# Optimization experiments

Hardware: AMD Instinct MI355X
Metric: run time of the kernel (lower is better)

## Reference

```python
import jax, jax.numpy as jnp
import numpy as np

B, W, H, C = 4, 32, 32, 128   # image feature map
S, D = 256, 512               # text seq len, text embed dim
NC = 64                       # num_channels (attention inner dim)


def setup_inputs() -> dict:
    key = jax.random.key(0)
    ks = jax.random.split(key, 16)
    def dense(k, din, dout):
        return jax.random.normal(k, (din, dout), jnp.float32) / np.sqrt(din)
    return {
        "x": jax.random.normal(ks[0], (B, W, H, C), jnp.float32),
        "s": jax.random.normal(ks[1], (B, S, D), jnp.float32),
        "a": jax.random.randint(ks[2], (B, S), 0, 2).astype(jnp.float32),
        "Wq": dense(ks[3], C, NC),  "bq": jnp.zeros((NC,), jnp.float32),
        "Wkx": dense(ks[4], C, NC), "bkx": jnp.zeros((NC,), jnp.float32),
        "Wvx": dense(ks[5], C, NC), "bvx": jnp.zeros((NC,), jnp.float32),
        "Wks": dense(ks[6], D, NC), "bks": jnp.zeros((NC,), jnp.float32),
        "Wvs": dense(ks[7], D, NC), "bvs": jnp.zeros((NC,), jnp.float32),
        "Wout": dense(ks[8], NC, C), "bout": jnp.zeros((C,), jnp.float32),
        "ln_scale": jnp.ones((C,), jnp.float32),
        "ln_bias": jnp.zeros((C,), jnp.float32),
    }


def reference(x, s, a, Wq, bq, Wkx, bkx, Wvx, bvx, Wks, bks, Wvs, bvs,
              Wout, bout, ln_scale, ln_bias):
    nc = Wq.shape[-1]
    # mask text embeddings: repeat(a,'b s -> b s d') * s
    te = s * a[:, :, None]
    # projections
    q = x @ Wq + bq            # (b,w,h,c)
    kx = x @ Wkx + bkx         # (b,w,h,c)
    vx = x @ Vx_dummy if False else x @ Wvx + bvx
    ks = te @ Wks + bks        # (b,s,c)
    vs = te @ Wvs + bvs        # (b,s,c)
    # broadcast-add spatial and text keys/values -> (b,w,h,s,c)
    k = kx[:, :, :, None, :] + ks[:, None, None, :, :]
    v = vx[:, :, :, None, :] + vs[:, None, None, :, :]
    # attention matrix over channels: v^T @ k contracted over s -> (b,w,h,c,c)
    attn = jnp.einsum('bwhsc,bwhsd->bwhcd', v, k) / jnp.sqrt(jnp.asarray(nc, x.dtype))
    attn = jax.nn.softmax(attn, axis=-1)
    # q applied through the channel-channel attention -> (b,w,h,c)
    out = jnp.einsum('bwhj,bwhjk->bwhk', q, attn)
    # output projection back to x channels, residual, layernorm
    out = out @ Wout + bout
    x = x + out
    mu = jnp.mean(x, axis=-1, keepdims=True)
    var = jnp.var(x, axis=-1, keepdims=True)
    x = (x - mu) * jax.lax.rsqrt(var + 1e-6) * ln_scale + ln_bias
    return x
```

## Files before the change

kernel.cpp:

```cpp
#include <hip/hip_runtime.h>
#include <hip/hip_bf16.h>

#define BB 4
#define SS 256
#define DD 512
#define CC 128
#define NC 64
#define PXB 4

__global__ __launch_bounds__(256) void fused_proj_kernel(
    const float* __restrict__ x,
    const float* __restrict__ Wq,  const float* __restrict__ bq,
    const float* __restrict__ Wkx, const float* __restrict__ bkx,
    const float* __restrict__ Wvx, const float* __restrict__ bvx,
    const float* __restrict__ s, const float* __restrict__ a,
    const float* __restrict__ Wks, const float* __restrict__ bks,
    const float* __restrict__ Wvs, const float* __restrict__ bvs,
    float* __restrict__ P, float* __restrict__ ksw, float* __restrict__ vsw)
{
    __shared__ float tel[2][DD];
    __shared__ float part[2][2][2][NC];
    __shared__ float xl[8][CC];

    const int t = threadIdx.x;
    const int w = t >> 6, lane = t & 63;

    if (blockIdx.x < 512) {
        const int px0 = blockIdx.x * 8;
        {
            const float4* x4 = (const float4*)(x + (size_t)px0 * CC);
            ((float4*)&xl[0][0])[t] = x4[t];
        }
        __syncthreads();
        if (w < 3) {
            const float* __restrict__ Wm = (w == 0) ? Wq : (w == 1 ? Wkx : Wvx);
            const float* __restrict__ bm = (w == 0) ? bq : (w == 1 ? bkx : bvx);
            const int ksub = lane >> 4;
            const int cg = (lane & 15) * 4;
            float4 acc[8] = {};
            #pragma unroll 4
            for (int j = 0; j < 32; ++j) {
                const int k = 4 * j + ksub;
                const float4 wv = *(const float4*)(Wm + (size_t)k * NC + cg);
                #pragma unroll
                for (int px = 0; px < 8; ++px) {
                    const float xv = xl[px][k];
                    acc[px].x = fmaf(xv, wv.x, acc[px].x);
                    acc[px].y = fmaf(xv, wv.y, acc[px].y);
                    acc[px].z = fmaf(xv, wv.z, acc[px].z);
                    acc[px].w = fmaf(xv, wv.w, acc[px].w);
                }
            }
            #pragma unroll
            for (int px = 0; px < 8; ++px) {
                #pragma unroll
                for (int off = 16; off <= 32; off <<= 1) {
                    acc[px].x += __shfl_down(acc[px].x, off);
                    acc[px].y += __shfl_down(acc[px].y, off);
                    acc[px].z += __shfl_down(acc[px].z, off);
                    acc[px].w += __shfl_down(acc[px].w, off);
                }
            }
            if (ksub == 0) {
                const float4 bb = *(const float4*)(bm + cg);
                #pragma unroll
                for (int px = 0; px < 8; ++px) {
                    float4 v;
                    v.x = acc[px].x + bb.x; v.y = acc[px].y + bb.y;
                    v.z = acc[px].z + bb.z; v.w = acc[px].w + bb.w;
                    *(float4*)(P + (size_t)(px0 + px) * 192 + w * 64 + cg) = v;
                }
            }
        }
    } else {
        const int row0 = (blockIdx.x - 512) * 2;
        {
            const float4* s4 = (const float4*)(s + (size_t)row0 * DD);
            const int r = t >> 7;
            const float am = a[row0 + r];
            float4 v = s4[t];
            v.x *= am; v.y *= am; v.z *= am; v.w *= am;
            ((float4*)&tel[0][0])[t] = v;
        }
        __syncthreads();

        const int m = w & 1, h = w >> 1;
        const int kb = h * 256;
        const int cg = (lane & 15) * 4;
        const int ksub = lane >> 4;
        const float* __restrict__ Wm = m ? Wvs : Wks;

        float4 acc0 = {0,0,0,0}, acc1 = {0,0,0,0};
        #pragma unroll 4
        for (int j = 0; j < 64; ++j) {
            const int k = kb + 4 * j + ksub;
            const float4 wv = *(const float4*)(Wm + (size_t)k * NC + cg);
            const float t0 = tel[0][k];
            const float t1 = tel[1][k];
            acc0.x = fmaf(t0, wv.x, acc0.x); acc0.y = fmaf(t0, wv.y, acc0.y);
            acc0.z = fmaf(t0, wv.z, acc0.z); acc0.w = fmaf(t0, wv.w, acc0.w);
            acc1.x = fmaf(t1, wv.x, acc1.x); acc1.y = fmaf(t1, wv.y, acc1.y);
            acc1.z = fmaf(t1, wv.z, acc1.z); acc1.w = fmaf(t1, wv.w, acc1.w);
        }
        #pragma unroll
        for (int off = 16; off <= 32; off <<= 1) {
            acc0.x += __shfl_down(acc0.x, off); acc0.y += __shfl_down(acc0.y, off);
            acc0.z += __shfl_down(acc0.z, off); acc0.w += __shfl_down(acc0.w, off);
            acc1.x += __shfl_down(acc1.x, off); acc1.y += __shfl_down(acc1.y, off);
            acc1.z += __shfl_down(acc1.z, off); acc1.w += __shfl_down(acc1.w, off);
        }
        if (lane < 16) {
            *(float4*)&part[m][h][0][cg] = acc0;
            *(float4*)&part[m][h][1][cg] = acc1;
        }
        __syncthreads();

        {
            const int mm = t >> 7, r = (t >> 6) & 1, col = t & 63;
            const float v = part[mm][0][r][col] + part[mm][1][r][col]
                          + (mm ? bvs[col] : bks[col]);
            float* dst = mm ? vsw : ksw;
            dst[(size_t)(row0 + r) * NC + col] = v;
        }
    }
}

__global__ __launch_bounds__(256) void reduce_kernel(
    const float* __restrict__ ksw, const float* __restrict__ vsw,
    float* __restrict__ Mw, float* __restrict__ Ksw, float* __restrict__ Vsw)
{
    __shared__ float pm[4][NC], pk[4][NC], pv[4];
    const int t = threadIdx.x, w = t >> 6, d = t & 63;
    const int b = blockIdx.x >> 6, c = blockIdx.x & 63;
    const float* __restrict__ vsb = vsw + (size_t)b * SS * NC;
    const float* __restrict__ ksb = ksw + (size_t)b * SS * NC;
    float acc = 0.f, ks_ = 0.f, vs_ = 0.f;
    #pragma unroll 4
    for (int j = 0; j < 64; ++j) {
        const int s2 = w * 64 + j;
        const float vv = vsb[s2 * NC + c];
        const float kv = ksb[s2 * NC + d];
        acc = fmaf(vv, kv, acc);
        ks_ += kv; vs_ += vv;
    }
    pm[w][d] = acc; pk[w][d] = ks_;
    if (d == 0) pv[w] = vs_;
    __syncthreads();
    if (t < 64) {
        Mw[((size_t)b * NC + c) * NC + t] = pm[0][t] + pm[1][t] + pm[2][t] + pm[3][t];
        if (c == 0) Ksw[b * NC + t] = pk[0][t] + pk[1][t] + pk[2][t] + pk[3][t];
        if (t == 0) Vsw[b * NC + c] = pv[0] + pv[1] + pv[2] + pv[3];
    }
}

__global__ __launch_bounds__(256) void pixel_kernel(
    const float* __restrict__ x, const float* __restrict__ P,
    const float* __restrict__ Wout, const float* __restrict__ bout,
    const float* __restrict__ ln_scale, const float* __restrict__ ln_bias,
    const float* __restrict__ Mw, const float* __restrict__ Ksw,
    const float* __restrict__ Vsw,
    float* __restrict__ out)
{
    __shared__ float Ml[NC * 65];
    __shared__ float projl[PXB][192];
    __shared__ float xl[PXB][CC];
    __shared__ float rsl[PXB][NC];
    __shared__ float mxl[PXB][NC];
    __shared__ float outl[PXB][NC];
    __shared__ float Ksl[NC], Vsl[NC];
    __shared__ float redl[2][2][4];

    const int t = threadIdx.x;
    const int w = t >> 6, lane = t & 63;
    const int px0g = blockIdx.x * PXB;
    const int b = px0g >> 10;

    {
        const float4* P4 = (const float4*)(P + (size_t)px0g * 192);
        for (int i = t; i < PXB * 192 / 4; i += 256)
            ((float4*)&projl[0][0])[i] = P4[i];
        const float4* x4 = (const float4*)(x + (size_t)px0g * CC);
        for (int i = t; i < PXB * CC / 4; i += 256)
            ((float4*)&xl[0][0])[i] = x4[i];
        const float* Mb = Mw + (size_t)b * NC * NC;
        for (int i = t; i < NC * NC; i += 256)
            Ml[(i >> 6) * 65 + (i & 63)] = Mb[i];
        if (t < NC) { Ksl[t] = Ksw[b * NC + t]; Vsl[t] = Vsw[b * NC + t]; }
    }
    __syncthreads();

    {
        const int px = w, c = lane;
        const float vxc = projl[px][128 + c];
        const float qc  = projl[px][c];
        const float uc  = fmaf(256.0f, vxc, Vsl[c]);
        float mx = -3.4e38f;
        #pragma unroll
        for (int d = 0; d < NC; ++d) {
            const float A = fmaf(uc, projl[px][64 + d],
                                 fmaf(vxc, Ksl[d], Ml[c * 65 + d])) * 0.125f;
            mx = fmaxf(mx, A);
        }
        float sum = 0.f;
        #pragma unroll
        for (int d = 0; d < NC; ++d) {
            const float A = fmaf(uc, projl[px][64 + d],
                                 fmaf(vxc, Ksl[d], Ml[c * 65 + d])) * 0.125f;
            sum += __expf(A - mx);
        }
        rsl[px][c] = qc / sum;
        mxl[px][c] = mx;
    }
    __syncthreads();

    {
        const int px = w, d = lane;
        const float kxd = projl[px][64 + d];
        const float Ksd = Ksl[d];
        float acc = 0.f;
        #pragma unroll 4
        for (int c = 0; c < NC; ++c) {
            const float vxc = projl[px][128 + c];
            const float uc = fmaf(256.0f, vxc, Vsl[c]);
            const float A = fmaf(uc, kxd, fmaf(vxc, Ksd, Ml[c * 65 + d])) * 0.125f;
            acc = fmaf(rsl[px][c], __expf(A - mxl[px][c]), acc);
        }
        outl[px][d] = acc;
    }
    __syncthreads();

    {
        const int col = t & 127;
        const int pxg = t >> 7;
        const int px0 = 2 * pxg, px1 = px0 + 1;
        float acc0 = 0.f, acc1 = 0.f;
        #pragma unroll 4
        for (int k = 0; k < NC; ++k) {
            const float wv = Wout[k * CC + col];
            acc0 = fmaf(outl[px0][k], wv, acc0);
            acc1 = fmaf(outl[px1][k], wv, acc1);
        }
        const float bb = bout[col];
        const float y0 = acc0 + bb + xl[px0][col];
        const float y1 = acc1 + bb + xl[px1][col];

        float s10 = y0, s20 = y0 * y0, s11 = y1, s21 = y1 * y1;
        #pragma unroll
        for (int off = 32; off >= 1; off >>= 1) {
            s10 += __shfl_down(s10, off);
            s20 += __shfl_down(s20, off);
            s11 += __shfl_down(s11, off);
            s21 += __shfl_down(s21, off);
        }
        const int half = (t >> 6) & 1;
        if (lane == 0) {
            redl[pxg][half][0] = s10; redl[pxg][half][1] = s20;
            redl[pxg][half][2] = s11; redl[pxg][half][3] = s21;
        }
        __syncthreads();
        const float S10 = redl[pxg][0][0] + redl[pxg][1][0];
        const float S20 = redl[pxg][0][1] + redl[pxg][1][1];
        const float S11 = redl[pxg][0][2] + redl[pxg][1][2];
        const float S21 = redl[pxg][0][3] + redl[pxg][1][3];
        const float mu0 = S10 * (1.f / 128.f);
        const float var0 = S20 * (1.f / 128.f) - mu0 * mu0;
        const float mu1 = S11 * (1.f / 128.f);
        const float var1 = S21 * (1.f / 128.f) - mu1 * mu1;
        const float r0 = rsqrtf(var0 + 1e-6f), r1 = rsqrtf(var1 + 1e-6f);
        const float gg = ln_scale[col], be = ln_bias[col];
        out[(size_t)(px0g + px0) * CC + col] = (y0 - mu0) * r0 * gg + be;
        out[(size_t)(px0g + px1) * CC + col] = (y1 - mu1) * r1 * gg + be;
    }
}

extern "C" void kernel_launch(void* const* d_in, const int* in_sizes, int n_in,
                              void* d_out, int out_size, void* d_ws, size_t ws_size,
                              hipStream_t stream) {
    const float* x        = (const float*)d_in[0];
    const float* s        = (const float*)d_in[1];
    const float* a        = (const float*)d_in[2];
    const float* Wq       = (const float*)d_in[3];
    const float* bq       = (const float*)d_in[4];
    const float* Wkx      = (const float*)d_in[5];
    const float* bkx      = (const float*)d_in[6];
    const float* Wvx      = (const float*)d_in[7];
    const float* bvx      = (const float*)d_in[8];
    const float* Wks      = (const float*)d_in[9];
    const float* bks      = (const float*)d_in[10];
    const float* Wvs      = (const float*)d_in[11];
    const float* bvs      = (const float*)d_in[12];
    const float* Wout     = (const float*)d_in[13];
    const float* bout     = (const float*)d_in[14];
    const float* ln_scale = (const float*)d_in[15];
    const float* ln_bias  = (const float*)d_in[16];

    float* ws  = (float*)d_ws;
    float* ksw = ws;
    float* vsw = ws + 65536;
    float* Mw  = ws + 131072;
    float* Ksw = ws + 147456;
    float* Vsw = ws + 147712;
    float* Pw  = ws + 147968;

    fused_proj_kernel<<<1024, 256, 0, stream>>>(
        x, Wq, bq, Wkx, bkx, Wvx, bvx, s, a, Wks, bks, Wvs, bvs, Pw, ksw, vsw);
    reduce_kernel<<<BB * NC, 256, 0, stream>>>(ksw, vsw, Mw, Ksw, Vsw);
    pixel_kernel<<<(BB * 1024) / PXB, 256, 0, stream>>>(
        x, Pw, Wout, bout, ln_scale, ln_bias, Mw, Ksw, Vsw, (float*)d_out);
}
```

Measured before the change: 117.1 us.

## Fuse pixel projections into pixel kernel and compute text M partials per block

The change restructures three launches into two. The text kernel now projects 16 text rows per block and writes partial M, Ks and Vs sums, which removes the separate reduce kernel. The pixel kernel computes q/kx/vx projections in shared memory, so the P workspace no longer goes through global memory, and it sums the 16 M partials itself. The costs are that every pixel block redundantly sums 16 partials of 64x64 floats, the text stage runs on only 64 blocks, and the pixel grid shrinks to 256 blocks of 1024 threads.

```diff
diff --git a/kernel.cpp b/kernel.cpp
--- a/kernel.cpp
+++ b/kernel.cpp
@@ -1,191 +1,204 @@
 #include <hip/hip_runtime.h>
-#include <hip/hip_bf16.h>
 
 #define BB 4
 #define SS 256
 #define DD 512
 #define CC 128
 #define NC 64
-#define PXB 4
-
-__global__ __launch_bounds__(256) void fused_proj_kernel(
+
+__global__ __launch_bounds__(512) void text_kernel(
+    const float* __restrict__ s, const float* __restrict__ a,
+    const float* __restrict__ Wks, const float* __restrict__ bks,
+    const float* __restrict__ Wvs, const float* __restrict__ bvs,
+    float* __restrict__ Mpart, float* __restrict__ Kspart,
+    float* __restrict__ Vspart)
+{
+    __shared__ float tel[16][DD];
+    __shared__ float ksl[16][NC];
+    __shared__ float vsl[16][NC];
+
+    const int t = threadIdx.x;
+    const int w = t >> 6, lane = t & 63;
+    const int b = blockIdx.x >> 4, q = blockIdx.x & 15;
+    const int srow0 = b * SS + q * 16;
+
+    {
+        const float4* s4 = (const float4*)(s + (size_t)srow0 * DD);
+        for (int i = t; i < 2048; i += 512) {
+            const int r = i >> 7;
+            const float am = a[srow0 + r];
+            float4 v = s4[i];
+            v.x *= am; v.y *= am; v.z *= am; v.w *= am;
+            ((float4*)&tel[0][0])[i] = v;
+        }
+    }
+    __syncthreads();
+
+    {
+        const int m = w & 1, rg = w >> 1;
+        const float* __restrict__ Wm = m ? Wvs : Wks;
+        const float* __restrict__ bm = m ? bvs : bks;
+        const int ksub = lane >> 4;
+        const int cg = (lane & 15) * 4;
+        float4 acc[4] = {};
+        #pragma unroll 4
+        for (int j = 0; j < 128; ++j) {
+            const int k = 4 * j + ksub;
+            const float4 wv = *(const float4*)(Wm + (size_t)k * NC + cg);
+            #pragma unroll
+            for (int r = 0; r < 4; ++r) {
+                const float tv = tel[rg * 4 + r][k];
+                acc[r].x = fmaf(tv, wv.x, acc[r].x);
+                acc[r].y = fmaf(tv, wv.y, acc[r].y);
+                acc[r].z = fmaf(tv, wv.z, acc[r].z);
+                acc[r].w = fmaf(tv, wv.w, acc[r].w);
+            }
+        }
+        #pragma unroll
+        for (int off = 16; off <= 32; off <<= 1) {
+            #pragma unroll
+            for (int r = 0; r < 4; ++r) {
+                acc[r].x += __shfl_down(acc[r].x, off);
+                acc[r].y += __shfl_down(acc[r].y, off);
+                acc[r].z += __shfl_down(acc[r].z, off);
+                acc[r].w += __shfl_down(acc[r].w, off);
+            }
+        }
+        if (ksub == 0) {
+            const float4 bb = *(const float4*)(bm + cg);
+            float (*dst)[NC] = m ? vsl : ksl;
+            #pragma unroll
+            for (int r = 0; r < 4; ++r) {
+                float4 v;
+                v.x = acc[r].x + bb.x; v.y = acc[r].y + bb.y;
+                v.z = acc[r].z + bb.z; v.w = acc[r].w + bb.w;
+                *(float4*)&dst[rg * 4 + r][cg] = v;
+            }
+        }
+    }
+    __syncthreads();
+
+    {
+        const int c = t >> 3;
+        const int d0 = (t & 7) * 8;
+        float4 A0 = {0,0,0,0}, A1 = {0,0,0,0};
+        #pragma unroll
+        for (int ss = 0; ss < 16; ++ss) {
+            const float vv = vsl[ss][c];
+            const float4 k0 = *(const float4*)&ksl[ss][d0];
+            const float4 k1 = *(const float4*)&ksl[ss][d0 + 4];
+            A0.x = fmaf(vv, k0.x, A0.x); A0.y = fmaf(vv, k0.y, A0.y);
+            A0.z = fmaf(vv, k0.z, A0.z); A0.w = fmaf(vv, k0.w, A0.w);
+            A1.x = fmaf(vv, k1.x, A1.x); A1.y = fmaf(vv, k1.y, A1.y);
+            A1.z = fmaf(vv, k1.z, A1.z); A1.w = fmaf(vv, k1.w, A1.w);
+        }
+        float* Mp = Mpart + ((size_t)(b * 16 + q)) * (NC * NC) + c * NC + d0;
+        *(float4*)Mp = A0;
+        *(float4*)(Mp + 4) = A1;
+    }
+    if (t < 128) {
+        const int m = t >> 6, d = t & 63;
+        const float (*src)[NC] = m ? vsl : ksl;
+        float sum = 0.f;
+        #pragma unroll
+        for (int ss = 0; ss < 16; ++ss) sum += src[ss][d];
+        float* dst = m ? Vspart : Kspart;
+        dst[(b * 16 + q) * NC + d] = sum;
+    }
+}
+
+__global__ __launch_bounds__(1024) void pixel_kernel(
     const float* __restrict__ x,
     const float* __restrict__ Wq,  const float* __restrict__ bq,
     const float* __restrict__ Wkx, const float* __restrict__ bkx,
     const float* __restrict__ Wvx, const float* __restrict__ bvx,
-    const float* __restrict__ s, const float* __restrict__ a,
-    const float* __restrict__ Wks, const float* __restrict__ bks,
-    const float* __restrict__ Wvs, const float* __restrict__ bvs,
-    float* __restrict__ P, float* __restrict__ ksw, float* __restrict__ vsw)
+    const float* __restrict__ Wout, const float* __restrict__ bout,
+    const float* __restrict__ ln_scale, const float* __restrict__ ln_bias,
+    const float* __restrict__ Mpart, const float* __restrict__ Kspart,
+    const float* __restrict__ Vspart,
+    float* __restrict__ out)
 {
-    __shared__ float tel[2][DD];
-    __shared__ float part[2][2][2][NC];
-    __shared__ float xl[8][CC];
+    __shared__ float Ml[NC * 65];
+    __shared__ float projl[16][192];
+    __shared__ float xl[16][CC];
+    __shared__ float rsl[16][NC];
+    __shared__ float mxl[16][NC];
+    __shared__ float outl[16][NC];
+    __shared__ float Ksl[NC], Vsl[NC];
+    __shared__ float redl[8][2][4];
 
     const int t = threadIdx.x;
     const int w = t >> 6, lane = t & 63;
-
-    if (blockIdx.x < 512) {
-        const int px0 = blockIdx.x * 8;
-        {
-            const float4* x4 = (const float4*)(x + (size_t)px0 * CC);
-            ((float4*)&xl[0][0])[t] = x4[t];
-        }
-        __syncthreads();
-        if (w < 3) {
-            const float* __restrict__ Wm = (w == 0) ? Wq : (w == 1 ? Wkx : Wvx);
-            const float* __restrict__ bm = (w == 0) ? bq : (w == 1 ? bkx : bvx);
+    const int px0g = blockIdx.x * 16;
+    const int b = blockIdx.x >> 6;
+
+    if (t < 512)
+        ((float4*)&xl[0][0])[t] = ((const float4*)(x + (size_t)px0g * CC))[t];
+
+    {
+        const float4* Mp4 = (const float4*)(Mpart + (size_t)b * 16 * (NC * NC));
+        float4 acc = {0,0,0,0};
+        #pragma unroll
+        for (int q = 0; q < 16; ++q) {
+            const float4 v = Mp4[q * 1024 + t];
+            acc.x += v.x; acc.y += v.y; acc.z += v.z; acc.w += v.w;
+        }
+        const int c = t >> 4, dq = t & 15;
+        float* dst = &Ml[c * 65 + dq * 4];
+        dst[0] = acc.x; dst[1] = acc.y; dst[2] = acc.z; dst[3] = acc.w;
+    }
+    if (t < 128) {
+        const int m = t >> 6, d = t & 63;
+        const float* Pp = (m ? Vspart : Kspart) + b * 16 * NC + d;
+        float sum = 0.f;
+        #pragma unroll
+        for (int q = 0; q < 16; ++q) sum += Pp[q * NC];
+        (m ? Vsl : Ksl)[d] = sum;
+    }
+    __syncthreads();
+
+    {
+        const int g = w >> 2, mg = w & 3;
+        if (mg < 3) {
+            const float* __restrict__ Wm = (mg == 0) ? Wq : (mg == 1 ? Wkx : Wvx);
+            const float* __restrict__ bm = (mg == 0) ? bq : (mg == 1 ? bkx : bvx);
             const int ksub = lane >> 4;
             const int cg = (lane & 15) * 4;
-            float4 acc[8] = {};
+            float4 acc[4] = {};
             #pragma unroll 4
             for (int j = 0; j < 32; ++j) {
                 const int k = 4 * j + ksub;
                 const float4 wv = *(const float4*)(Wm + (size_t)k * NC + cg);
                 #pragma unroll
-                for (int px = 0; px < 8; ++px) {
-                    const float xv = xl[px][k];
-                    acc[px].x = fmaf(xv, wv.x, acc[px].x);
-                    acc[px].y = fmaf(xv, wv.y, acc[px].y);
-                    acc[px].z = fmaf(xv, wv.z, acc[px].z);
-                    acc[px].w = fmaf(xv, wv.w, acc[px].w);
+                for (int p = 0; p < 4; ++p) {
+                    const float xv = xl[g * 4 + p][k];
+                    acc[p].x = fmaf(xv, wv.x, acc[p].x);
+                    acc[p].y = fmaf(xv, wv.y, acc[p].y);
+                    acc[p].z = fmaf(xv, wv.z, acc[p].z);
+                    acc[p].w = fmaf(xv, wv.w, acc[p].w);
                 }
             }
             #pragma unroll
-            for (int px = 0; px < 8; ++px) {
+            for (int p = 0; p < 4; ++p) {
                 #pragma unroll
                 for (int off = 16; off <= 32; off <<= 1) {
-                    acc[px].x += __shfl_down(acc[px].x, off);
-                    acc[px].y += __shfl_down(acc[px].y, off);
-                    acc[px].z += __shfl_down(acc[px].z, off);
-                    acc[px].w += __shfl_down(acc[px].w, off);
+                    acc[p].x += __shfl_down(acc[p].x, off);
+                    acc[p].y += __shfl_down(acc[p].y, off);
+                    acc[p].z += __shfl_down(acc[p].z, off);
+                    acc[p].w += __shfl_down(acc[p].w, off);
                 }
             }
             if (ksub == 0) {
                 const float4 bb = *(const float4*)(bm + cg);
                 #pragma unroll
-                for (int px = 0; px < 8; ++px) {
+                for (int p = 0; p < 4; ++p) {
                     float4 v;
-                    v.x = acc[px].x + bb.x; v.y = acc[px].y + bb.y;
-                    v.z = acc[px].z + bb.z; v.w = acc[px].w + bb.w;
-                    *(float4*)(P + (size_t)(px0 + px) * 192 + w * 64 + cg) = v;
+                    v.x = acc[p].x + bb.x; v.y = acc[p].y + bb.y;
+                    v.z = acc[p].z + bb.z; v.w = acc[p].w + bb.w;
+                    *(float4*)&projl[g * 4 + p][mg * 64 + cg] = v;
                 }
             }
         }
-    } else {
-        const int row0 = (blockIdx.x - 512) * 2;
-        {
-            const float4* s4 = (const float4*)(s + (size_t)row0 * DD);
-            const int r = t >> 7;
-            const float am = a[row0 + r];
-            float4 v = s4[t];
-            v.x *= am; v.y *= am; v.z *= am; v.w *= am;
-            ((float4*)&tel[0][0])[t] = v;
-        }
-        __syncthreads();
-
-        const int m = w & 1, h = w >> 1;
-        const int kb = h * 256;
-        const int cg = (lane & 15) * 4;
-        const int ksub = lane >> 4;
-        const float* __restrict__ Wm = m ? Wvs : Wks;
-
-        float4 acc0 = {0,0,0,0}, acc1 = {0,0,0,0};
-        #pragma unroll 4
-        for (int j = 0; j < 64; ++j) {
-            const int k = kb + 4 * j + ksub;
-            const float4 wv = *(const float4*)(Wm + (size_t)k * NC + cg);
-            const float t0 = tel[0][k];
-            const float t1 = tel[1][k];
-            acc0.x = fmaf(t0, wv.x, acc0.x); acc0.y = fmaf(t0, wv.y, acc0.y);
-            acc0.z = fmaf(t0, wv.z, acc0.z); acc0.w = fmaf(t0, wv.w, acc0.w);
-            acc1.x = fmaf(t1, wv.x, acc1.x); acc1.y = fmaf(t1, wv.y, acc1.y);
-            acc1.z = fmaf(t1, wv.z, acc1.z); acc1.w = fmaf(t1, wv.w, acc1.w);
-        }
-        #pragma unroll
-        for (int off = 16; off <= 32; off <<= 1) {
-            acc0.x += __shfl_down(acc0.x, off); acc0.y += __shfl_down(acc0.y, off);
-            acc0.z += __shfl_down(acc0.z, off); acc0.w += __shfl_down(acc0.w, off);
-            acc1.x += __shfl_down(acc1.x, off); acc1.y += __shfl_down(acc1.y, off);
-            acc1.z += __shfl_down(acc1.z, off); acc1.w += __shfl_down(acc1.w, off);
-        }
-        if (lane < 16) {
-            *(float4*)&part[m][h][0][cg] = acc0;
-            *(float4*)&part[m][h][1][cg] = acc1;
-        }
-        __syncthreads();
-
-        {
-            const int mm = t >> 7, r = (t >> 6) & 1, col = t & 63;
-            const float v = part[mm][0][r][col] + part[mm][1][r][col]
-                          + (mm ? bvs[col] : bks[col]);
-            float* dst = mm ? vsw : ksw;
-            dst[(size_t)(row0 + r) * NC + col] = v;
-        }
-    }
-}
-
-__global__ __launch_bounds__(256) void reduce_kernel(
-    const float* __restrict__ ksw, const float* __restrict__ vsw,
-    float* __restrict__ Mw, float* __restrict__ Ksw, float* __restrict__ Vsw)
-{
-    __shared__ float pm[4][NC], pk[4][NC], pv[4];
-    const int t = threadIdx.x, w = t >> 6, d = t & 63;
-    const int b = blockIdx.x >> 6, c = blockIdx.x & 63;
-    const float* __restrict__ vsb = vsw + (size_t)b * SS * NC;
-    const float* __restrict__ ksb = ksw + (size_t)b * SS * NC;
-    float acc = 0.f, ks_ = 0.f, vs_ = 0.f;
-    #pragma unroll 4
-    for (int j = 0; j < 64; ++j) {
-        const int s2 = w * 64 + j;
-        const float vv = vsb[s2 * NC + c];
-        const float kv = ksb[s2 * NC + d];
-        acc = fmaf(vv, kv, acc);
-        ks_ += kv; vs_ += vv;
-    }
-    pm[w][d] = acc; pk[w][d] = ks_;
-    if (d == 0) pv[w] = vs_;
-    __syncthreads();
-    if (t < 64) {
-        Mw[((size_t)b * NC + c) * NC + t] = pm[0][t] + pm[1][t] + pm[2][t] + pm[3][t];
-        if (c == 0) Ksw[b * NC + t] = pk[0][t] + pk[1][t] + pk[2][t] + pk[3][t];
-        if (t == 0) Vsw[b * NC + c] = pv[0] + pv[1] + pv[2] + pv[3];
-    }
-}
-
-__global__ __launch_bounds__(256) void pixel_kernel(
-    const float* __restrict__ x, const float* __restrict__ P,
-    const float* __restrict__ Wout, const float* __restrict__ bout,
-    const float* __restrict__ ln_scale, const float* __restrict__ ln_bias,
-    const float* __restrict__ Mw, const float* __restrict__ Ksw,
-    const float* __restrict__ Vsw,
-    float* __restrict__ out)
-{
-    __shared__ float Ml[NC * 65];
-    __shared__ float projl[PXB][192];
-    __shared__ float xl[PXB][CC];
-    __shared__ float rsl[PXB][NC];
-    __shared__ float mxl[PXB][NC];
-    __shared__ float outl[PXB][NC];
-    __shared__ float Ksl[NC], Vsl[NC];
-    __shared__ float redl[2][2][4];
-
-    const int t = threadIdx.x;
-    const int w = t >> 6, lane = t & 63;
-    const int px0g = blockIdx.x * PXB;
-    const int b = px0g >> 10;
-
-    {
-        const float4* P4 = (const float4*)(P + (size_t)px0g * 192);
-        for (int i = t; i < PXB * 192 / 4; i += 256)
-            ((float4*)&projl[0][0])[i] = P4[i];
-        const float4* x4 = (const float4*)(x + (size_t)px0g * CC);
-        for (int i = t; i < PXB * CC / 4; i += 256)
-            ((float4*)&xl[0][0])[i] = x4[i];
-        const float* Mb = Mw + (size_t)b * NC * NC;
-        for (int i = t; i < NC * NC; i += 256)
-            Ml[(i >> 6) * 65 + (i & 63)] = Mb[i];
-        if (t < NC) { Ksl[t] = Ksw[b * NC + t]; Vsl[t] = Vsw[b * NC + t]; }
     }
     __syncthreads();
 
@@ -294,17 +307,14 @@
     const float* ln_scale = (const float*)d_in[15];
     const float* ln_bias  = (const float*)d_in[16];
 
-    float* ws  = (float*)d_ws;
-    float* ksw = ws;
-    float* vsw = ws + 65536;
-    float* Mw  = ws + 131072;
-    float* Ksw = ws + 147456;
-    float* Vsw = ws + 147712;
-    float* Pw  = ws + 147968;
-
-    fused_proj_kernel<<<1024, 256, 0, stream>>>(
-        x, Wq, bq, Wkx, bkx, Wvx, bvx, s, a, Wks, bks, Wvs, bvs, Pw, ksw, vsw);
-    reduce_kernel<<<BB * NC, 256, 0, stream>>>(ksw, vsw, Mw, Ksw, Vsw);
-    pixel_kernel<<<(BB * 1024) / PXB, 256, 0, stream>>>(
-        x, Pw, Wout, bout, ln_scale, ln_bias, Mw, Ksw, Vsw, (float*)d_out);
+    float* ws     = (float*)d_ws;
+    float* Mpart  = ws;
+    float* Kspart = ws + 262144;
+    float* Vspart = ws + 266240;
+
+    text_kernel<<<64, 512, 0, stream>>>(
+        s, a, Wks, bks, Wvs, bvs, Mpart, Kspart, Vspart);
+    pixel_kernel<<<256, 1024, 0, stream>>>(
+        x, Wq, bq, Wkx, bkx, Wvx, bvx, Wout, bout, ln_scale, ln_bias,
+        Mpart, Kspart, Vspart, (float*)d_out);
 }
```

New measurement: 123.5 us. 1.05x slower.
